# Optimization experiments

Measured on AMD Instinct MI355X. Metric: run time of the kernel, lower is better.

## Reference

```python
import jax, jax.numpy as jnp
import numpy as np

N = 8192
F_IN = 256
F_OUT = 128
ALPHA = 0.2  # LeakyReLU negative slope (cfg.model.gat_alpha)


def setup_inputs() -> dict:
    key = jax.random.key(0)
    k1, k2, k3, k4 = jax.random.split(key, 4)
    inp = jax.random.normal(k1, (N, F_IN), dtype=jnp.float32)
    adj = jax.random.randint(k2, (N, N), 0, 2, dtype=jnp.int32)
    # xavier_uniform with gain=1.414
    gain = 1.414
    limW = gain * np.sqrt(6.0 / (F_IN + F_OUT))
    W = jax.random.uniform(k3, (F_IN, F_OUT), minval=-limW, maxval=limW, dtype=jnp.float32)
    lima = gain * np.sqrt(6.0 / (2 * F_OUT + 1))
    a = jax.random.uniform(k4, (2 * F_OUT, 1), minval=-lima, maxval=lima, dtype=jnp.float32)
    return {"input": inp, "adj": adj, "W": W, "a": a}


def reference(input, adj, W, a):
    h = input @ W                     # [N, F_OUT]
    a1 = a[:F_OUT, 0]                 # score contribution of source node i
    a2 = a[F_OUT:, 0]                 # score contribution of target node j
    # e[i, j] = leakyrelu(a1.h_i + a2.h_j)  -- same math as the NxN concat
    s1 = h @ a1                       # [N]
    s2 = h @ a2                       # [N]
    e = jax.nn.leaky_relu(s1[:, None] + s2[None, :], negative_slope=ALPHA)  # [N, N]
    attention = jnp.where(adj > 0, e, jnp.float32(-9e15))
    attention = jax.nn.softmax(attention, axis=1)
    # dropout p=0 / eval mode -> no-op
    h_prime = attention @ h           # [N, F_OUT]
    return jax.nn.elu(h_prime)        # concat=True branch
```

## Files before the change

### kernel.cpp

```cpp
#include <hip/hip_runtime.h>
#include <hip/hip_bf16.h>

#define N 8192
#define FIN 256
#define FOUT 128
#define ALPHA 0.2f

typedef unsigned short ushort_t;
typedef __attribute__((ext_vector_type(8))) short short8;
typedef __attribute__((ext_vector_type(4))) float f32x4;

#define GLOAD16(gp, lp)                                        \
  __builtin_amdgcn_global_load_lds(                            \
      (const __attribute__((address_space(1))) void*)(gp),     \
      (__attribute__((address_space(3))) void*)(lp), 16, 0, 0)

__device__ __forceinline__ ushort_t f2bf(float x) {
  __hip_bfloat16 b = __float2bfloat16(x);
  return *reinterpret_cast<ushort_t*>(&b);
}

__global__ __launch_bounds__(256) void k_h(const float* __restrict__ inp,
                                           const float* __restrict__ Wm,
                                           const float* __restrict__ av,
                                           ushort_t* __restrict__ hT,
                                           float* __restrict__ s1,
                                           float* __restrict__ s2) {
  __shared__ float in_lds[16][FIN];
  __shared__ float h_tile[16][FOUT];
  const int t = threadIdx.x;
  const int r0 = blockIdx.x * 16;

  for (int idx = t; idx < 16 * FIN; idx += 256) {
    int ii = idx >> 8, kk = idx & 255;
    in_lds[ii][kk] = inp[(size_t)(r0 + ii) * FIN + kk];
  }
  __syncthreads();

  const int c2 = (t & 63) * 2;
  const int rg = t >> 6;
  float acc[4][2] = {};
  for (int k = 0; k < FIN; k += 4) {
    float4 iv[4];
#pragma unroll
    for (int q = 0; q < 4; ++q)
      iv[q] = *reinterpret_cast<const float4*>(&in_lds[rg * 4 + q][k]);
#pragma unroll
    for (int kk = 0; kk < 4; ++kk) {
      float2 wp = *reinterpret_cast<const float2*>(&Wm[(size_t)(k + kk) * FOUT + c2]);
#pragma unroll
      for (int q = 0; q < 4; ++q) {
        float x = reinterpret_cast<const float*>(&iv[q])[kk];
        acc[q][0] = fmaf(x, wp.x, acc[q][0]);
        acc[q][1] = fmaf(x, wp.y, acc[q][1]);
      }
    }
  }
#pragma unroll
  for (int q = 0; q < 4; ++q) {
    h_tile[rg * 4 + q][c2] = acc[q][0];
    h_tile[rg * 4 + q][c2 + 1] = acc[q][1];
  }
  __syncthreads();

  const int wv_ = t >> 6, lane = t & 63;
#pragma unroll
  for (int rr = 0; rr < 4; ++rr) {
    int row = wv_ * 4 + rr;
    float h0 = h_tile[row][lane], h1 = h_tile[row][lane + 64];
    float p1 = h0 * av[lane] + h1 * av[lane + 64];
    float p2 = h0 * av[FOUT + lane] + h1 * av[FOUT + lane + 64];
#pragma unroll
    for (int m = 32; m; m >>= 1) {
      p1 += __shfl_xor(p1, m);
      p2 += __shfl_xor(p2, m);
    }
    if (lane == 0) { s1[r0 + row] = p1; s2[r0 + row] = p2; }
  }

  for (int idx = t; idx < 16 * FOUT; idx += 256) {
    int c = idx >> 4, ii = idx & 15;
    hT[(size_t)c * N + r0 + ii] = f2bf(h_tile[ii][c]);
  }
}

__global__ __launch_bounds__(256) void k_smax(const float* __restrict__ s2,
                                              float* __restrict__ outm) {
  __shared__ float red[4];
  const int t = threadIdx.x;
  float m = -1e30f;
  for (int i = t; i < N; i += 256) m = fmaxf(m, s2[i]);
#pragma unroll
  for (int d = 32; d; d >>= 1) m = fmaxf(m, __shfl_xor(m, d));
  if ((t & 63) == 0) red[t >> 6] = m;
  __syncthreads();
  if (t == 0) outm[0] = fmaxf(fmaxf(red[0], red[1]), fmaxf(red[2], red[3]));
}

__global__ __launch_bounds__(512, 4) void k_attn(const int* __restrict__ adj,
                                                 const ushort_t* __restrict__ hT,
                                                 const float* __restrict__ s1g,
                                                 const float* __restrict__ s2g,
                                                 const float* __restrict__ s2max,
                                                 float* __restrict__ slab,
                                                 float* __restrict__ denp,
                                                 int jc, int ntiles) {
  __shared__ __align__(16) ushort_t Bt[32768];
  __shared__ float Dred[8][16];

  const int t = threadIdx.x;
  const int lane = t & 63;
  const int wid = t >> 6;
  const int rb = blockIdx.x & 127;
  const int chunk = blockIdx.x >> 7;
  const int i0 = rb * 64;
  const int jc0 = chunk * jc;

  const int g = wid & 3;
  const int hf = wid >> 2;
  const int arow = lane & 15;
  const int kb = lane >> 4;
  const int irow = i0 + g * 16 + arow;

  const float s1v = s1g[irow];
  const float mraw = s1v + s2max[0];
  const float mv = mraw > 0.f ? mraw : ALPHA * mraw;
  const float L2E = 1.44269504f;
  const float mvl = mv * L2E;

  const int* __restrict__ adjp = adj + (size_t)irow * N + jc0 + hf * 128 + kb * 8;
  const float* __restrict__ s2p = s2g + jc0 + hf * 128 + kb * 8;
  const char* __restrict__ hTb = (const char*)hT;

  f32x4 acc[8];
#pragma unroll
  for (int ct = 0; ct < 8; ++ct) acc[ct] = (f32x4){0.f, 0.f, 0.f, 0.f};
  float dacc = 0.f;

  for (int jt = 0; jt < ntiles; ++jt) {
    const int j0 = jt * 256;

#pragma unroll
    for (int s = 0; s < 8; ++s) {
      int L = s * 512 + t;
      int row = L >> 5;
      int boff = (L & 31) * 16;
      const char* src = hTb + ((size_t)row * N + jc0 + j0) * 2 + (boff ^ ((row & 7) << 4));
      GLOAD16(src, (char*)Bt + L * 16);
    }

    int4 a0[4], a1[4];
#pragma unroll
    for (int kq = 0; kq < 4; ++kq) {
      a0[kq] = *reinterpret_cast<const int4*>(adjp + j0 + kq * 32);
      a1[kq] = *reinterpret_cast<const int4*>(adjp + j0 + kq * 32 + 4);
    }

    __syncthreads();

#pragma unroll
    for (int kq = 0; kq < 4; ++kq) {
      short8 bf[8];
      const int byte0 = hf * 256 + kq * 64 + kb * 16;
#pragma unroll
      for (int ct = 0; ct < 8; ++ct) {
        int row = ct * 16 + arow;
        int off = row * 512 + (byte0 ^ ((row & 7) << 4));
        bf[ct] = *reinterpret_cast<const short8*>((const char*)Bt + off);
      }
      float4 sv0 = *reinterpret_cast<const float4*>(s2p + j0 + kq * 32);
      float4 sv1 = *reinterpret_cast<const float4*>(s2p + j0 + kq * 32 + 4);
      const int* ai0 = reinterpret_cast<const int*>(&a0[kq]);
      const int* ai1 = reinterpret_cast<const int*>(&a1[kq]);
      const float* sf0 = reinterpret_cast<const float*>(&sv0);
      const float* sf1 = reinterpret_cast<const float*>(&sv1);
      short8 af;
#pragma unroll
      for (int e = 0; e < 4; ++e) {
        float pre = s1v + sf0[e];
        float lr = fmaxf(pre, ALPHA * pre);
        float w = __builtin_amdgcn_exp2f(fmaf(lr, L2E, -mvl));
        w = (ai0[e] > 0) ? w : 0.f;
        dacc += w;
        af[e] = (short)f2bf(w);
      }
#pragma unroll
      for (int e = 0; e < 4; ++e) {
        float pre = s1v + sf1[e];
        float lr = fmaxf(pre, ALPHA * pre);
        float w = __builtin_amdgcn_exp2f(fmaf(lr, L2E, -mvl));
        w = (ai1[e] > 0) ? w : 0.f;
        dacc += w;
        af[4 + e] = (short)f2bf(w);
      }
#pragma unroll
      for (int ct = 0; ct < 8; ++ct)
        acc[ct] = __builtin_amdgcn_mfma_f32_16x16x32_bf16(af, bf[ct], acc[ct], 0, 0, 0);
    }

    __syncthreads();
  }

  dacc += __shfl_xor(dacc, 16);
  dacc += __shfl_xor(dacc, 32);
  if (lane < 16) Dred[wid][lane] = dacc;

  float (*Hred)[132] = (float(*)[132])(void*)Bt;
  if (hf == 0) {
#pragma unroll
    for (int ct = 0; ct < 8; ++ct)
#pragma unroll
      for (int r = 0; r < 4; ++r)
        Hred[g * 16 + kb * 4 + r][ct * 16 + arow] = acc[ct][r];
  }
  __syncthreads();
  if (hf == 1) {
#pragma unroll
    for (int ct = 0; ct < 8; ++ct)
#pragma unroll
      for (int r = 0; r < 4; ++r)
        Hred[g * 16 + kb * 4 + r][ct * 16 + arow] += acc[ct][r];
  }
  __syncthreads();

  if (t < 64)
    denp[(size_t)chunk * N + i0 + t] = Dred[t >> 4][t & 15] + Dred[(t >> 4) + 4][t & 15];

  for (int idx = t; idx < 64 * 128; idx += 512) {
    int r = idx >> 7, c = idx & 127;
    slab[((size_t)chunk * N + i0 + r) * 128 + c] = Hred[r][c];
  }
}

__global__ __launch_bounds__(256) void k_fin(const float* __restrict__ slab,
                                             const float* __restrict__ denp,
                                             float* __restrict__ out, int nchunks) {
  const int idx = blockIdx.x * 256 + threadIdx.x;
  const int i = idx >> 7;
  float den = 0.f, v = 0.f;
  for (int k = 0; k < nchunks; ++k) {
    den += denp[(size_t)k * N + i];
    v += slab[(size_t)k * N * FOUT + idx];
  }
  v /= den;
  out[idx] = v > 0.f ? v : (__expf(v) - 1.f);
}

extern "C" void kernel_launch(void* const* d_in, const int* in_sizes, int n_in,
                              void* d_out, int out_size, void* d_ws, size_t ws_size,
                              hipStream_t stream) {
  const float* inp = (const float*)d_in[0];
  const int* adj   = (const int*)d_in[1];
  const float* Wm  = (const float*)d_in[2];
  const float* av  = (const float*)d_in[3];
  float* out = (float*)d_out;

  char* ws = (char*)d_ws;
  ushort_t* hT = (ushort_t*)ws;
  float* s1    = (float*)(ws + (size_t)FOUT * N * 2);
  float* s2    = s1 + N;
  float* s2mx  = s2 + N;
  float* slab  = s2mx + 4;

  const size_t base = (size_t)FOUT * N * 2 + (size_t)N * 4 * 2 + 16;
  int nchunks = 4;
  while (nchunks > 1) {
    size_t need = base + (size_t)nchunks * N * FOUT * 4 + (size_t)nchunks * N * 4;
    if (need <= ws_size) break;
    nchunks >>= 1;
  }
  float* denp = slab + (size_t)nchunks * N * FOUT;
  const int jc = N / nchunks;
  const int ntiles = jc / 256;

  k_h<<<N / 16, 256, 0, stream>>>(inp, Wm, av, hT, s1, s2);
  k_smax<<<1, 256, 0, stream>>>(s2, s2mx);
  k_attn<<<128 * nchunks, 512, 0, stream>>>(adj, hT, s1, s2, s2mx, slab, denp, jc, ntiles);
  k_fin<<<(N * FOUT) / 256, 256, 0, stream>>>(slab, denp, out, nchunks);
}
```

Measured before the change: 125.7 us.

## Pack adjacency into a bitmask before the attention kernel

```diff
diff --git a/kernel.cpp b/kernel.cpp
--- a/kernel.cpp
+++ b/kernel.cpp
@@ -18,6 +18,27 @@
 __device__ __forceinline__ ushort_t f2bf(float x) {
   __hip_bfloat16 b = __float2bfloat16(x);
   return *reinterpret_cast<ushort_t*>(&b);
+}
+
+__global__ __launch_bounds__(256) void k_pack(const int* __restrict__ adj,
+                                              unsigned char* __restrict__ mask) {
+  const size_t tid = (size_t)blockIdx.x * 256 + threadIdx.x;
+  const size_t nthr = (size_t)gridDim.x * 256;
+  const size_t total = (size_t)N * N / 8;
+  for (size_t b = tid; b < total; b += nthr) {
+    const int4* p = reinterpret_cast<const int4*>(adj + b * 8);
+    int4 v0 = p[0], v1 = p[1];
+    unsigned m = 0;
+    m |= (v0.x > 0) ? 1u : 0u;
+    m |= (v0.y > 0) ? 2u : 0u;
+    m |= (v0.z > 0) ? 4u : 0u;
+    m |= (v0.w > 0) ? 8u : 0u;
+    m |= (v1.x > 0) ? 16u : 0u;
+    m |= (v1.y > 0) ? 32u : 0u;
+    m |= (v1.z > 0) ? 64u : 0u;
+    m |= (v1.w > 0) ? 128u : 0u;
+    mask[b] = (unsigned char)m;
+  }
 }
 
 __global__ __launch_bounds__(256) void k_h(const float* __restrict__ inp,
@@ -97,7 +118,7 @@
   if (t == 0) outm[0] = fmaxf(fmaxf(red[0], red[1]), fmaxf(red[2], red[3]));
 }
 
-__global__ __launch_bounds__(512, 4) void k_attn(const int* __restrict__ adj,
+__global__ __launch_bounds__(512, 4) void k_attn(const unsigned int* __restrict__ mask,
                                                  const ushort_t* __restrict__ hT,
                                                  const float* __restrict__ s1g,
                                                  const float* __restrict__ s2g,
@@ -128,7 +149,8 @@
   const float L2E = 1.44269504f;
   const float mvl = mv * L2E;
 
-  const int* __restrict__ adjp = adj + (size_t)irow * N + jc0 + hf * 128 + kb * 8;
+  const unsigned int* __restrict__ maskp =
+      mask + (size_t)irow * (N / 32) + ((jc0 + hf * 128) >> 5);
   const float* __restrict__ s2p = s2g + jc0 + hf * 128 + kb * 8;
   const char* __restrict__ hTb = (const char*)hT;
 
@@ -149,12 +171,7 @@
       GLOAD16(src, (char*)Bt + L * 16);
     }
 
-    int4 a0[4], a1[4];
-#pragma unroll
-    for (int kq = 0; kq < 4; ++kq) {
-      a0[kq] = *reinterpret_cast<const int4*>(adjp + j0 + kq * 32);
-      a1[kq] = *reinterpret_cast<const int4*>(adjp + j0 + kq * 32 + 4);
-    }
+    int4 mw = *reinterpret_cast<const int4*>(maskp + (j0 >> 5));
 
     __syncthreads();
 
@@ -168,10 +185,11 @@
         int off = row * 512 + (byte0 ^ ((row & 7) << 4));
         bf[ct] = *reinterpret_cast<const short8*>((const char*)Bt + off);
       }
+      const unsigned w8 =
+          (((unsigned)(kq == 0 ? mw.x : kq == 1 ? mw.y : kq == 2 ? mw.z : mw.w)) >>
+           (kb * 8)) & 0xffu;
       float4 sv0 = *reinterpret_cast<const float4*>(s2p + j0 + kq * 32);
       float4 sv1 = *reinterpret_cast<const float4*>(s2p + j0 + kq * 32 + 4);
-      const int* ai0 = reinterpret_cast<const int*>(&a0[kq]);
-      const int* ai1 = reinterpret_cast<const int*>(&a1[kq]);
       const float* sf0 = reinterpret_cast<const float*>(&sv0);
       const float* sf1 = reinterpret_cast<const float*>(&sv1);
       short8 af;
@@ -180,7 +198,7 @@
         float pre = s1v + sf0[e];
         float lr = fmaxf(pre, ALPHA * pre);
         float w = __builtin_amdgcn_exp2f(fmaf(lr, L2E, -mvl));
-        w = (ai0[e] > 0) ? w : 0.f;
+        w = ((w8 >> e) & 1u) ? w : 0.f;
         dacc += w;
         af[e] = (short)f2bf(w);
       }
@@ -189,7 +207,7 @@
         float pre = s1v + sf1[e];
         float lr = fmaxf(pre, ALPHA * pre);
         float w = __builtin_amdgcn_exp2f(fmaf(lr, L2E, -mvl));
-        w = (ai1[e] > 0) ? w : 0.f;
+        w = ((w8 >> (4 + e)) & 1u) ? w : 0.f;
         dacc += w;
         af[4 + e] = (short)f2bf(w);
       }
@@ -260,9 +278,10 @@
   float* s1    = (float*)(ws + (size_t)FOUT * N * 2);
   float* s2    = s1 + N;
   float* s2mx  = s2 + N;
-  float* slab  = s2mx + 4;
-
-  const size_t base = (size_t)FOUT * N * 2 + (size_t)N * 4 * 2 + 16;
+  unsigned char* mask = (unsigned char*)(s2mx + 4);
+  float* slab  = (float*)(mask + (size_t)N * N / 8);
+
+  const size_t base = (size_t)FOUT * N * 2 + (size_t)N * 4 * 2 + 16 + (size_t)N * N / 8;
   int nchunks = 4;
   while (nchunks > 1) {
     size_t need = base + (size_t)nchunks * N * FOUT * 4 + (size_t)nchunks * N * 4;
@@ -273,8 +292,10 @@
   const int jc = N / nchunks;
   const int ntiles = jc / 256;
 
+  k_pack<<<2048, 256, 0, stream>>>(adj, mask);
   k_h<<<N / 16, 256, 0, stream>>>(inp, Wm, av, hT, s1, s2);
   k_smax<<<1, 256, 0, stream>>>(s2, s2mx);
-  k_attn<<<128 * nchunks, 512, 0, stream>>>(adj, hT, s1, s2, s2mx, slab, denp, jc, ntiles);
+  k_attn<<<128 * nchunks, 512, 0, stream>>>((const unsigned int*)mask, hT, s1, s2,
+                                            s2mx, slab, denp, jc, ntiles);
   k_fin<<<(N * FOUT) / 256, 256, 0, stream>>>(slab, denp, out, nchunks);
 }
```

Measured after the change: 121.5 us. 3.3% less time.

## Double-buffer hT tiles and prefetch adjacency as packed LDS bitmask

Applied to the files above, without the earlier changes.

```diff
diff --git a/kernel.cpp b/kernel.cpp
--- a/kernel.cpp
+++ b/kernel.cpp
@@ -97,15 +97,16 @@
   if (t == 0) outm[0] = fmaxf(fmaxf(red[0], red[1]), fmaxf(red[2], red[3]));
 }
 
-__global__ __launch_bounds__(512, 4) void k_attn(const int* __restrict__ adj,
-                                                 const ushort_t* __restrict__ hT,
-                                                 const float* __restrict__ s1g,
-                                                 const float* __restrict__ s2g,
-                                                 const float* __restrict__ s2max,
-                                                 float* __restrict__ slab,
-                                                 float* __restrict__ denp,
-                                                 int jc, int ntiles) {
-  __shared__ __align__(16) ushort_t Bt[32768];
+__global__ __launch_bounds__(512) void k_attn(const int* __restrict__ adj,
+                                              const ushort_t* __restrict__ hT,
+                                              const float* __restrict__ s1g,
+                                              const float* __restrict__ s2g,
+                                              const float* __restrict__ s2max,
+                                              float* __restrict__ slab,
+                                              float* __restrict__ denp,
+                                              int jc, int ntiles) {
+  __shared__ __align__(16) ushort_t Bt[2][32768];
+  __shared__ unsigned mask_lds[2][64][8];
   __shared__ float Dred[8][16];
 
   const int t = threadIdx.x;
@@ -128,36 +129,60 @@
   const float L2E = 1.44269504f;
   const float mvl = mv * L2E;
 
-  const int* __restrict__ adjp = adj + (size_t)irow * N + jc0 + hf * 128 + kb * 8;
+  const int ar_ = t >> 3, aq = t & 7;
+  const int* __restrict__ adjq = adj + (size_t)(i0 + ar_) * N + jc0 + aq * 32;
+
   const float* __restrict__ s2p = s2g + jc0 + hf * 128 + kb * 8;
   const char* __restrict__ hTb = (const char*)hT;
 
+#define STAGE_HT(J0, BUF)                                                          \
+  _Pragma("unroll") for (int s = 0; s < 8; ++s) {                                  \
+    int L = s * 512 + t;                                                           \
+    int rr = L >> 5;                                                               \
+    int boff = (L & 31) * 16;                                                      \
+    const char* src =                                                              \
+        hTb + ((size_t)rr * N + jc0 + (J0)) * 2 + (boff ^ ((rr & 7) << 4));        \
+    GLOAD16(src, (char*)(&Bt[BUF][0]) + L * 16);                                   \
+  }
+
+#define LOAD_ADJ(J0)                                                               \
+  _Pragma("unroll") for (int s = 0; s < 8; ++s)                                    \
+      ar[s] = *reinterpret_cast<const int4*>(adjq + (J0) + s * 4);
+
+#define PACK_MASK(BUF)                                                             \
+  {                                                                                \
+    unsigned w = 0;                                                                \
+    _Pragma("unroll") for (int s = 0; s < 8; ++s) {                                \
+      w |= (ar[s].x > 0 ? 1u : 0u) << (s * 4);                                     \
+      w |= (ar[s].y > 0 ? 1u : 0u) << (s * 4 + 1);                                 \
+      w |= (ar[s].z > 0 ? 1u : 0u) << (s * 4 + 2);                                 \
+      w |= (ar[s].w > 0 ? 1u : 0u) << (s * 4 + 3);                                 \
+    }                                                                              \
+    mask_lds[BUF][ar_][aq] = w;                                                    \
+  }
+
   f32x4 acc[8];
 #pragma unroll
   for (int ct = 0; ct < 8; ++ct) acc[ct] = (f32x4){0.f, 0.f, 0.f, 0.f};
   float dacc = 0.f;
+  int4 ar[8];
+
+  LOAD_ADJ(0)
+  STAGE_HT(0, 0)
+  PACK_MASK(0)
+  __syncthreads();
 
   for (int jt = 0; jt < ntiles; ++jt) {
-    const int j0 = jt * 256;
-
-#pragma unroll
-    for (int s = 0; s < 8; ++s) {
-      int L = s * 512 + t;
-      int row = L >> 5;
-      int boff = (L & 31) * 16;
-      const char* src = hTb + ((size_t)row * N + jc0 + j0) * 2 + (boff ^ ((row & 7) << 4));
-      GLOAD16(src, (char*)Bt + L * 16);
+    const int b = jt & 1;
+    const bool pf = (jt + 1) < ntiles;
+
+    if (pf) {
+      LOAD_ADJ((jt + 1) * 256)
+      STAGE_HT((jt + 1) * 256, b ^ 1)
     }
 
-    int4 a0[4], a1[4];
-#pragma unroll
-    for (int kq = 0; kq < 4; ++kq) {
-      a0[kq] = *reinterpret_cast<const int4*>(adjp + j0 + kq * 32);
-      a1[kq] = *reinterpret_cast<const int4*>(adjp + j0 + kq * 32 + 4);
-    }
-
-    __syncthreads();
-
+    const char* btb = (const char*)(&Bt[b][0]);
+    const unsigned* mrow = &mask_lds[b][g * 16 + arow][0];
 #pragma unroll
     for (int kq = 0; kq < 4; ++kq) {
       short8 bf[8];
@@ -166,12 +191,11 @@
       for (int ct = 0; ct < 8; ++ct) {
         int row = ct * 16 + arow;
         int off = row * 512 + (byte0 ^ ((row & 7) << 4));
-        bf[ct] = *reinterpret_cast<const short8*>((const char*)Bt + off);
+        bf[ct] = *reinterpret_cast<const short8*>(btb + off);
       }
-      float4 sv0 = *reinterpret_cast<const float4*>(s2p + j0 + kq * 32);
-      float4 sv1 = *reinterpret_cast<const float4*>(s2p + j0 + kq * 32 + 4);
-      const int* ai0 = reinterpret_cast<const int*>(&a0[kq]);
-      const int* ai1 = reinterpret_cast<const int*>(&a1[kq]);
+      const unsigned w8 = (mrow[hf * 4 + kq] >> (kb * 8)) & 0xffu;
+      float4 sv0 = *reinterpret_cast<const float4*>(s2p + jt * 256 + kq * 32);
+      float4 sv1 = *reinterpret_cast<const float4*>(s2p + jt * 256 + kq * 32 + 4);
       const float* sf0 = reinterpret_cast<const float*>(&sv0);
       const float* sf1 = reinterpret_cast<const float*>(&sv1);
       short8 af;
@@ -180,7 +204,7 @@
         float pre = s1v + sf0[e];
         float lr = fmaxf(pre, ALPHA * pre);
         float w = __builtin_amdgcn_exp2f(fmaf(lr, L2E, -mvl));
-        w = (ai0[e] > 0) ? w : 0.f;
+        w = ((w8 >> e) & 1u) ? w : 0.f;
         dacc += w;
         af[e] = (short)f2bf(w);
       }
@@ -189,7 +213,7 @@
         float pre = s1v + sf1[e];
         float lr = fmaxf(pre, ALPHA * pre);
         float w = __builtin_amdgcn_exp2f(fmaf(lr, L2E, -mvl));
-        w = (ai1[e] > 0) ? w : 0.f;
+        w = ((w8 >> (4 + e)) & 1u) ? w : 0.f;
         dacc += w;
         af[4 + e] = (short)f2bf(w);
       }
@@ -198,8 +222,13 @@
         acc[ct] = __builtin_amdgcn_mfma_f32_16x16x32_bf16(af, bf[ct], acc[ct], 0, 0, 0);
     }
 
+    if (pf) PACK_MASK(b ^ 1)
+
     __syncthreads();
   }
+#undef STAGE_HT
+#undef LOAD_ADJ
+#undef PACK_MASK
 
   dacc += __shfl_xor(dacc, 16);
   dacc += __shfl_xor(dacc, 32);
@@ -262,13 +291,7 @@
   float* s2mx  = s2 + N;
   float* slab  = s2mx + 4;
 
-  const size_t base = (size_t)FOUT * N * 2 + (size_t)N * 4 * 2 + 16;
-  int nchunks = 4;
-  while (nchunks > 1) {
-    size_t need = base + (size_t)nchunks * N * FOUT * 4 + (size_t)nchunks * N * 4;
-    if (need <= ws_size) break;
-    nchunks >>= 1;
-  }
+  const int nchunks = 2;
   float* denp = slab + (size_t)nchunks * N * FOUT;
   const int jc = N / nchunks;
   const int ntiles = jc / 256;
```

Result: slower. 128.8 us (+2.4%).

## Prepack adjacency into bitmask and factor exponentials into per-row/column products

Applied to the files above, without the earlier changes.

```diff
diff --git a/kernel.cpp b/kernel.cpp
--- a/kernel.cpp
+++ b/kernel.cpp
@@ -20,17 +20,39 @@
   return *reinterpret_cast<ushort_t*>(&b);
 }
 
-__global__ __launch_bounds__(256) void k_h(const float* __restrict__ inp,
-                                           const float* __restrict__ Wm,
-                                           const float* __restrict__ av,
-                                           ushort_t* __restrict__ hT,
-                                           float* __restrict__ s1,
-                                           float* __restrict__ s2) {
+__global__ __launch_bounds__(256) void k_fh(const float* __restrict__ inp,
+                                            const float* __restrict__ Wm,
+                                            const float* __restrict__ av,
+                                            const int* __restrict__ adj,
+                                            ushort_t* __restrict__ hT,
+                                            float* __restrict__ s1,
+                                            float* __restrict__ s2,
+                                            unsigned* __restrict__ maskRM) {
   __shared__ float in_lds[16][FIN];
   __shared__ float h_tile[16][FOUT];
   const int t = threadIdx.x;
+
+  if (blockIdx.x >= 512) {
+    const size_t tid = (size_t)(blockIdx.x - 512) * 256 + t;
+    const size_t nthr = (size_t)(gridDim.x - 512) * 256;
+    const size_t nwords = (size_t)N * (N / 32);
+    for (size_t w = tid; w < nwords; w += nthr) {
+      const int4* p = reinterpret_cast<const int4*>(adj + w * 32);
+      unsigned m = 0;
+#pragma unroll
+      for (int s = 0; s < 8; ++s) {
+        int4 v = p[s];
+        m |= (v.x > 0 ? 1u : 0u) << (s * 4);
+        m |= (v.y > 0 ? 1u : 0u) << (s * 4 + 1);
+        m |= (v.z > 0 ? 1u : 0u) << (s * 4 + 2);
+        m |= (v.w > 0 ? 1u : 0u) << (s * 4 + 3);
+      }
+      maskRM[w] = m;
+    }
+    return;
+  }
+
   const int r0 = blockIdx.x * 16;
-
   for (int idx = t; idx < 16 * FIN; idx += 256) {
     int ii = idx >> 8, kk = idx & 255;
     in_lds[ii][kk] = inp[(size_t)(r0 + ii) * FIN + kk];
@@ -97,11 +119,25 @@
   if (t == 0) outm[0] = fmaxf(fmaxf(red[0], red[1]), fmaxf(red[2], red[3]));
 }
 
-__global__ __launch_bounds__(512, 4) void k_attn(const int* __restrict__ adj,
+__global__ __launch_bounds__(256) void k_coef(const float* __restrict__ s1,
+                                              const float* __restrict__ s2,
+                                              const float* __restrict__ s2max,
+                                              float2* __restrict__ QS,
+                                              float2* __restrict__ PR) {
+  const int i = blockIdx.x * 256 + threadIdx.x;
+  const float smx = s2max[0];
+  float s1v = s1[i];
+  float pre = s1v + smx;
+  float mv = pre > 0.f ? pre : ALPHA * pre;
+  PR[i] = make_float2(__expf(s1v - mv), __expf(ALPHA * s1v - mv));
+  float s2v = s2[i];
+  QS[i] = make_float2(__expf(s2v), __expf(ALPHA * s2v));
+}
+
+__global__ __launch_bounds__(512, 4) void k_attn(const unsigned* __restrict__ maskRM,
                                                  const ushort_t* __restrict__ hT,
-                                                 const float* __restrict__ s1g,
-                                                 const float* __restrict__ s2g,
-                                                 const float* __restrict__ s2max,
+                                                 const float2* __restrict__ QS,
+                                                 const float2* __restrict__ PR,
                                                  float* __restrict__ slab,
                                                  float* __restrict__ denp,
                                                  int jc, int ntiles) {
@@ -122,14 +158,12 @@
   const int kb = lane >> 4;
   const int irow = i0 + g * 16 + arow;
 
-  const float s1v = s1g[irow];
-  const float mraw = s1v + s2max[0];
-  const float mv = mraw > 0.f ? mraw : ALPHA * mraw;
-  const float L2E = 1.44269504f;
-  const float mvl = mv * L2E;
-
-  const int* __restrict__ adjp = adj + (size_t)irow * N + jc0 + hf * 128 + kb * 8;
-  const float* __restrict__ s2p = s2g + jc0 + hf * 128 + kb * 8;
+  const float2 pr = PR[irow];
+  const float Pv = pr.x, Rv = pr.y;
+
+  const unsigned* __restrict__ maskp =
+      maskRM + (size_t)irow * (N / 32) + ((jc0 + hf * 128) >> 5);
+  const float2* __restrict__ qsp = QS + jc0 + hf * 128 + kb * 8;
   const char* __restrict__ hTb = (const char*)hT;
 
   f32x4 acc[8];
@@ -143,18 +177,14 @@
 #pragma unroll
     for (int s = 0; s < 8; ++s) {
       int L = s * 512 + t;
-      int row = L >> 5;
+      int rr = L >> 5;
       int boff = (L & 31) * 16;
-      const char* src = hTb + ((size_t)row * N + jc0 + j0) * 2 + (boff ^ ((row & 7) << 4));
+      const char* src =
+          hTb + ((size_t)rr * N + jc0 + j0) * 2 + (boff ^ ((rr & 7) << 4));
       GLOAD16(src, (char*)Bt + L * 16);
     }
 
-    int4 a0[4], a1[4];
-#pragma unroll
-    for (int kq = 0; kq < 4; ++kq) {
-      a0[kq] = *reinterpret_cast<const int4*>(adjp + j0 + kq * 32);
-      a1[kq] = *reinterpret_cast<const int4*>(adjp + j0 + kq * 32 + 4);
-    }
+    int4 mw = *reinterpret_cast<const int4*>(maskp + (j0 >> 5));
 
     __syncthreads();
 
@@ -168,31 +198,21 @@
         int off = row * 512 + (byte0 ^ ((row & 7) << 4));
         bf[ct] = *reinterpret_cast<const short8*>((const char*)Bt + off);
       }
-      float4 sv0 = *reinterpret_cast<const float4*>(s2p + j0 + kq * 32);
-      float4 sv1 = *reinterpret_cast<const float4*>(s2p + j0 + kq * 32 + 4);
-      const int* ai0 = reinterpret_cast<const int*>(&a0[kq]);
-      const int* ai1 = reinterpret_cast<const int*>(&a1[kq]);
-      const float* sf0 = reinterpret_cast<const float*>(&sv0);
-      const float* sf1 = reinterpret_cast<const float*>(&sv1);
+      const unsigned word = (kq == 0) ? mw.x : (kq == 1) ? mw.y : (kq == 2) ? mw.z : mw.w;
+      const unsigned w8 = (word >> (kb * 8)) & 0xffu;
+      const float4* q4 = reinterpret_cast<const float4*>(qsp + j0 + kq * 32);
+      float4 qa = q4[0], qb = q4[1], qc = q4[2], qd = q4[3];
       short8 af;
-#pragma unroll
-      for (int e = 0; e < 4; ++e) {
-        float pre = s1v + sf0[e];
-        float lr = fmaxf(pre, ALPHA * pre);
-        float w = __builtin_amdgcn_exp2f(fmaf(lr, L2E, -mvl));
-        w = (ai0[e] > 0) ? w : 0.f;
-        dacc += w;
-        af[e] = (short)f2bf(w);
-      }
-#pragma unroll
-      for (int e = 0; e < 4; ++e) {
-        float pre = s1v + sf1[e];
-        float lr = fmaxf(pre, ALPHA * pre);
-        float w = __builtin_amdgcn_exp2f(fmaf(lr, L2E, -mvl));
-        w = (ai1[e] > 0) ? w : 0.f;
-        dacc += w;
-        af[4 + e] = (short)f2bf(w);
-      }
+      float w;
+      w = fmaxf(Pv * qa.x, Rv * qa.y); w = (w8 & 1u) ? w : 0.f; dacc += w; af[0] = (short)f2bf(w);
+      w = fmaxf(Pv * qa.z, Rv * qa.w); w = (w8 & 2u) ? w : 0.f; dacc += w; af[1] = (short)f2bf(w);
+      w = fmaxf(Pv * qb.x, Rv * qb.y); w = (w8 & 4u) ? w : 0.f; dacc += w; af[2] = (short)f2bf(w);
+      w = fmaxf(Pv * qb.z, Rv * qb.w); w = (w8 & 8u) ? w : 0.f; dacc += w; af[3] = (short)f2bf(w);
+      w = fmaxf(Pv * qc.x, Rv * qc.y); w = (w8 & 16u) ? w : 0.f; dacc += w; af[4] = (short)f2bf(w);
+      w = fmaxf(Pv * qc.z, Rv * qc.w); w = (w8 & 32u) ? w : 0.f; dacc += w; af[5] = (short)f2bf(w);
+      w = fmaxf(Pv * qd.x, Rv * qd.y); w = (w8 & 64u) ? w : 0.f; dacc += w; af[6] = (short)f2bf(w);
+      w = fmaxf(Pv * qd.z, Rv * qd.w); w = (w8 & 128u) ? w : 0.f; dacc += w; af[7] = (short)f2bf(w);
+
 #pragma unroll
       for (int ct = 0; ct < 8; ++ct)
         acc[ct] = __builtin_amdgcn_mfma_f32_16x16x32_bf16(af, bf[ct], acc[ct], 0, 0, 0);
@@ -260,10 +280,14 @@
   float* s1    = (float*)(ws + (size_t)FOUT * N * 2);
   float* s2    = s1 + N;
   float* s2mx  = s2 + N;
-  float* slab  = s2mx + 4;
-
-  const size_t base = (size_t)FOUT * N * 2 + (size_t)N * 4 * 2 + 16;
-  int nchunks = 4;
+  float2* QS   = (float2*)(s2mx + 4);
+  float2* PR   = QS + N;
+  unsigned* maskRM = (unsigned*)(PR + N);
+  float* slab  = (float*)(maskRM + (size_t)N * N / 32);
+
+  const size_t base = (size_t)FOUT * N * 2 + (size_t)N * 4 * 2 + 16 +
+                      (size_t)N * 16 + (size_t)N * N / 8;
+  int nchunks = 2;
   while (nchunks > 1) {
     size_t need = base + (size_t)nchunks * N * FOUT * 4 + (size_t)nchunks * N * 4;
     if (need <= ws_size) break;
@@ -273,8 +297,9 @@
   const int jc = N / nchunks;
   const int ntiles = jc / 256;
 
-  k_h<<<N / 16, 256, 0, stream>>>(inp, Wm, av, hT, s1, s2);
+  k_fh<<<2048, 256, 0, stream>>>(inp, Wm, av, adj, hT, s1, s2, maskRM);
   k_smax<<<1, 256, 0, stream>>>(s2, s2mx);
-  k_attn<<<128 * nchunks, 512, 0, stream>>>(adj, hT, s1, s2, s2mx, slab, denp, jc, ntiles);
+  k_coef<<<N / 256, 256, 0, stream>>>(s1, s2, s2mx, QS, PR);
+  k_attn<<<128 * nchunks, 512, 0, stream>>>(maskRM, hT, QS, PR, slab, denp, jc, ntiles);
   k_fin<<<(N * FOUT) / 256, 256, 0, stream>>>(slab, denp, out, nchunks);
 }
```

Measured after the change: 172.2 us. 1.37x slower.
